# Optimization experiments

Measured on AMD Instinct MI355X. Metric: run time of the kernel, lower is better.

Reference implementation:

```python
import jax, jax.numpy as jnp
import numpy as np

IN_DIM, D_MODEL, HIDDEN, N_BLOCKS, N_CLASSES = 784, 16, 6, 4, 10
BATCH = 65536


def setup_inputs() -> dict:
    key = jax.random.key(0)
    ks = jax.random.split(key, 6)
    std = 0.02
    x = jax.random.normal(ks[0], (BATCH, IN_DIM), dtype=jnp.float32)
    # nn.Linear stores weight as [out, in]; we keep that convention.
    W_embed = jax.random.normal(ks[1], (D_MODEL, IN_DIM), dtype=jnp.float32) * std
    L_w = jax.random.normal(ks[2], (N_BLOCKS, HIDDEN, D_MODEL), dtype=jnp.float32) * std
    R_w = jax.random.normal(ks[3], (N_BLOCKS, HIDDEN, D_MODEL), dtype=jnp.float32) * std
    D_w = jax.random.normal(ks[4], (N_BLOCKS, D_MODEL, HIDDEN), dtype=jnp.float32) * std
    W_head = jax.random.normal(ks[5], (N_CLASSES, D_MODEL), dtype=jnp.float32) * std
    return {"x": x, "W_embed": W_embed, "L_w": L_w, "R_w": R_w, "D_w": D_w, "W_head": W_head}


def reference(x, W_embed, L_w, R_w, D_w, W_head):
    # embed: [B, in_dim] @ [in_dim, d_model]
    h_x = x @ W_embed.T  # [B, d_model]
    all_h = []
    for i in range(N_BLOCKS):  # n_blocks is a small structural constant
        u = h_x @ L_w[i].T  # [B, hidden]
        v = h_x @ R_w[i].T  # [B, hidden]
        h = u * v
        h_x = h_x + h @ D_w[i].T  # residual
        all_h.append(h)
    logits = h_x @ W_head.T  # [B, n_classes]
    return (logits, *all_h)
```

## Files before the change

kernel.cpp:

```cpp
#include <hip/hip_runtime.h>


#define IN_DIM   784
#define D_MODEL  16
#define HIDDEN   6
#define N_BLOCKS 4
#define N_CLS    10
#define BATCH    65536
#define SEG      196
#define NIT      49

__global__ __launch_bounds__(256, 4) void bilinear_resnet_fused(
    const float* __restrict__ x,
    const float* __restrict__ W_embed,
    const float* __restrict__ L_w,
    const float* __restrict__ R_w,
    const float* __restrict__ D_w,
    const float* __restrict__ W_head,
    float* __restrict__ out)
{
    __shared__ float parts[3][64][17];

    const int tid  = threadIdx.x;
    const int lane = tid & 63;
    const int wv   = __builtin_amdgcn_readfirstlane(tid >> 6);
    const int row  = blockIdx.x * 64 + lane;

    const float4* xr = reinterpret_cast<const float4*>(
        x + (size_t)row * IN_DIM + wv * SEG);
    const float* wseg = W_embed + wv * SEG;

    float acc[D_MODEL];
#pragma unroll
    for (int d = 0; d < D_MODEL; ++d) acc[d] = 0.f;

    float4 cur = xr[0];
    for (int it = 0; it < NIT; ++it) {
        float4 nxt = make_float4(0.f, 0.f, 0.f, 0.f);
        if (it + 1 < NIT) nxt = xr[it + 1];
        const float* wk = wseg + it * 4;
#pragma unroll
        for (int d = 0; d < D_MODEL; ++d) {
            const float* wd = wk + d * IN_DIM;
            float s = acc[d];
            s = fmaf(cur.x, wd[0], s);
            s = fmaf(cur.y, wd[1], s);
            s = fmaf(cur.z, wd[2], s);
            s = fmaf(cur.w, wd[3], s);
            acc[d] = s;
        }
        cur = nxt;
    }

    if (wv != 0) {
#pragma unroll
        for (int d = 0; d < D_MODEL; ++d) parts[wv - 1][lane][d] = acc[d];
    }
    __syncthreads();
    if (wv != 0) return;

#pragma unroll
    for (int d = 0; d < D_MODEL; ++d)
        acc[d] += parts[0][lane][d] + parts[1][lane][d] + parts[2][lane][d];

#pragma unroll
    for (int b = 0; b < N_BLOCKS; ++b) {
        const float* Lb = L_w + b * HIDDEN * D_MODEL;
        const float* Rb = R_w + b * HIDDEN * D_MODEL;
        const float* Db = D_w + b * D_MODEL * HIDDEN;
        float h[HIDDEN];
#pragma unroll
        for (int j = 0; j < HIDDEN; ++j) {
            float u = 0.f, v = 0.f;
#pragma unroll
            for (int d = 0; d < D_MODEL; ++d) {
                u = fmaf(acc[d], Lb[j * D_MODEL + d], u);
                v = fmaf(acc[d], Rb[j * D_MODEL + d], v);
            }
            h[j] = u * v;
        }
#pragma unroll
        for (int d = 0; d < D_MODEL; ++d) {
            float s = acc[d];
#pragma unroll
            for (int j = 0; j < HIDDEN; ++j) s = fmaf(h[j], Db[d * HIDDEN + j], s);
            acc[d] = s;
        }
        float* hout = out + (size_t)N_CLS * BATCH + (size_t)b * HIDDEN * BATCH
                      + (size_t)row * HIDDEN;
#pragma unroll
        for (int j = 0; j < HIDDEN; ++j) hout[j] = h[j];
    }

    float* lout = out + (size_t)row * N_CLS;
#pragma unroll
    for (int k = 0; k < N_CLS; ++k) {
        float s = 0.f;
#pragma unroll
        for (int d = 0; d < D_MODEL; ++d) s = fmaf(acc[d], W_head[k * D_MODEL + d], s);
        lout[k] = s;
    }
}

extern "C" void kernel_launch(void* const* d_in, const int* in_sizes, int n_in,
                              void* d_out, int out_size, void* d_ws, size_t ws_size,
                              hipStream_t stream) {
    const float* x       = (const float*)d_in[0];
    const float* W_embed = (const float*)d_in[1];
    const float* L_w     = (const float*)d_in[2];
    const float* R_w     = (const float*)d_in[3];
    const float* D_w     = (const float*)d_in[4];
    const float* W_head  = (const float*)d_in[5];
    float* out = (float*)d_out;

    const int grid = BATCH / 64;
    bilinear_resnet_fused<<<grid, 256, 0, stream>>>(
        x, W_embed, L_w, R_w, D_w, W_head, out);
}
```

Baseline: 354.2 us.

## Stage x tiles through swizzled shared memory with coalesced double-buffered loads

Replaces the per-thread strided row reads of x, where each lane read a 196-float segment of its own row, with cooperative coalesced float4 loads of 64x64 chunks into an XOR-swizzled, double-buffered LDS tile. Each wave then consumes a 16-column slice of every chunk from shared memory. The final 16 columns are read directly from global memory. The aim is better DRAM coalescing on this memory-bound embedding, at the cost of a __syncthreads per chunk and 32KB of LDS per block, which may reduce occupancy.

```diff
diff --git a/kernel.cpp b/kernel.cpp
--- a/kernel.cpp
+++ b/kernel.cpp
@@ -7,8 +7,7 @@
 #define N_BLOCKS 4
 #define N_CLS    10
 #define BATCH    65536
-#define SEG      196
-#define NIT      49
+#define NCHUNK   12
 
 __global__ __launch_bounds__(256, 4) void bilinear_resnet_fused(
     const float* __restrict__ x,
@@ -19,49 +18,99 @@
     const float* __restrict__ W_head,
     float* __restrict__ out)
 {
-    __shared__ float parts[3][64][17];
+    __shared__ float4 buf[2][64 * 16];
 
     const int tid  = threadIdx.x;
     const int lane = tid & 63;
     const int wv   = __builtin_amdgcn_readfirstlane(tid >> 6);
     const int row  = blockIdx.x * 64 + lane;
 
-    const float4* xr = reinterpret_cast<const float4*>(
-        x + (size_t)row * IN_DIM + wv * SEG);
-    const float* wseg = W_embed + wv * SEG;
+    const float* xtile = x + (size_t)blockIdx.x * 64 * IN_DIM;
 
     float acc[D_MODEL];
 #pragma unroll
     for (int d = 0; d < D_MODEL; ++d) acc[d] = 0.f;
 
-    float4 cur = xr[0];
-    for (int it = 0; it < NIT; ++it) {
-        float4 nxt = make_float4(0.f, 0.f, 0.f, 0.f);
-        if (it + 1 < NIT) nxt = xr[it + 1];
-        const float* wk = wseg + it * 4;
+    int lr[4], lk[4];
+#pragma unroll
+    for (int it = 0; it < 4; ++it) {
+        int i = it * 256 + tid;
+        lr[it] = i >> 4;
+        lk[it] = i & 15;
+    }
+
+    float4 pf[4];
+#pragma unroll
+    for (int it = 0; it < 4; ++it)
+        pf[it] = *reinterpret_cast<const float4*>(
+            xtile + (size_t)lr[it] * IN_DIM + lk[it] * 4);
+#pragma unroll
+    for (int it = 0; it < 4; ++it)
+        buf[0][lr[it] * 16 + (lk[it] ^ (lr[it] & 15))] = pf[it];
+    __syncthreads();
+
+    for (int c = 0; c < NCHUNK; ++c) {
+        if (c + 1 < NCHUNK) {
+#pragma unroll
+            for (int it = 0; it < 4; ++it)
+                pf[it] = *reinterpret_cast<const float4*>(
+                    xtile + (size_t)lr[it] * IN_DIM + (c + 1) * 64 + lk[it] * 4);
+        }
+        const float* wc = W_embed + c * 64 + wv * 16;
+        const float4* bsrc = buf[c & 1];
+#pragma unroll
+        for (int j = 0; j < 4; ++j) {
+            const int kk = wv * 4 + j;
+            const float4 xv = bsrc[lane * 16 + (kk ^ (lane & 15))];
+#pragma unroll
+            for (int d = 0; d < D_MODEL; ++d) {
+                const float* wd = wc + d * IN_DIM + j * 4;
+                float s = acc[d];
+                s = fmaf(xv.x, wd[0], s);
+                s = fmaf(xv.y, wd[1], s);
+                s = fmaf(xv.z, wd[2], s);
+                s = fmaf(xv.w, wd[3], s);
+                acc[d] = s;
+            }
+        }
+        if (c + 1 < NCHUNK) {
+#pragma unroll
+            for (int it = 0; it < 4; ++it)
+                buf[(c + 1) & 1][lr[it] * 16 + (lk[it] ^ (lr[it] & 15))] = pf[it];
+        }
+        __syncthreads();
+    }
+
+    {
+        const float4 xv = *reinterpret_cast<const float4*>(
+            x + (size_t)row * IN_DIM + 768 + wv * 4);
+        const float* wt = W_embed + 768 + wv * 4;
 #pragma unroll
         for (int d = 0; d < D_MODEL; ++d) {
-            const float* wd = wk + d * IN_DIM;
+            const float* wd = wt + d * IN_DIM;
             float s = acc[d];
-            s = fmaf(cur.x, wd[0], s);
-            s = fmaf(cur.y, wd[1], s);
-            s = fmaf(cur.z, wd[2], s);
-            s = fmaf(cur.w, wd[3], s);
+            s = fmaf(xv.x, wd[0], s);
+            s = fmaf(xv.y, wd[1], s);
+            s = fmaf(xv.z, wd[2], s);
+            s = fmaf(xv.w, wd[3], s);
             acc[d] = s;
         }
-        cur = nxt;
     }
 
+    float* parts = reinterpret_cast<float*>(&buf[0][0]);
     if (wv != 0) {
 #pragma unroll
-        for (int d = 0; d < D_MODEL; ++d) parts[wv - 1][lane][d] = acc[d];
+        for (int d = 0; d < D_MODEL; ++d)
+            parts[((wv - 1) * 64 + lane) * 17 + d] = acc[d];
     }
     __syncthreads();
     if (wv != 0) return;
 
 #pragma unroll
     for (int d = 0; d < D_MODEL; ++d)
-        acc[d] += parts[0][lane][d] + parts[1][lane][d] + parts[2][lane][d];
+        acc[d] += parts[(0 * 64 + lane) * 17 + d]
+                + parts[(1 * 64 + lane) * 17 + d]
+                + parts[(2 * 64 + lane) * 17 + d];
 
 #pragma unroll
     for (int b = 0; b < N_BLOCKS; ++b) {
```

Measured after the change: 364.4 us. +2.9%, slower.

## Compute embedding GEMM with bf16 MFMA and async double-buffered LDS staging

Applied to the files above, without the earlier changes.

Replaces the per-thread scalar FMA embedding, which split K across four waves, with an MFMA 16x16x32 bf16 matrix multiply. Each wave now owns 16 rows. The x tile is streamed into LDS with global_load_lds in double-buffered 64-column chunks using an XOR swizzle, and W_embed is converted to bf16 once per block into LDS. It also vectorizes the h and logits stores as float2. Rounding inputs to bf16 lowers precision, and each block re-converts W_embed on entry.

```diff
diff --git a/kernel.cpp b/kernel.cpp
--- a/kernel.cpp
+++ b/kernel.cpp
@@ -7,10 +7,22 @@
 #define N_BLOCKS 4
 #define N_CLS    10
 #define BATCH    65536
-#define SEG      196
-#define NIT      49
-
-__global__ __launch_bounds__(256, 4) void bilinear_resnet_fused(
+#define KC       64
+#define NCH      12
+#define WPITCH   808
+
+typedef const __attribute__((address_space(1))) void gvoid_t;
+typedef __attribute__((address_space(3))) void svoid_t;
+typedef __attribute__((ext_vector_type(8))) short bf16x8;
+typedef __attribute__((ext_vector_type(4))) float f32x4;
+
+__device__ __forceinline__ short f2bf(float f) {
+    unsigned u = __builtin_bit_cast(unsigned, f);
+    unsigned r = (u + 0x7FFFu + ((u >> 16) & 1u)) >> 16;
+    return (short)r;
+}
+
+__global__ __launch_bounds__(256, 2) void bilinear_resnet_fused(
     const float* __restrict__ x,
     const float* __restrict__ W_embed,
     const float* __restrict__ L_w,
@@ -19,49 +31,113 @@
     const float* __restrict__ W_head,
     float* __restrict__ out)
 {
-    __shared__ float parts[3][64][17];
+    __shared__ float4 xbuf[2][64 * 16];
+    __shared__ short  Wlds[16 * WPITCH];
+    __shared__ float4 xtail[64 * 4];
+    __shared__ float  hx[64 * 20];
 
     const int tid  = threadIdx.x;
     const int lane = tid & 63;
     const int wv   = __builtin_amdgcn_readfirstlane(tid >> 6);
-    const int row  = blockIdx.x * 64 + lane;
-
-    const float4* xr = reinterpret_cast<const float4*>(
-        x + (size_t)row * IN_DIM + wv * SEG);
-    const float* wseg = W_embed + wv * SEG;
-
-    float acc[D_MODEL];
-#pragma unroll
-    for (int d = 0; d < D_MODEL; ++d) acc[d] = 0.f;
-
-    float4 cur = xr[0];
-    for (int it = 0; it < NIT; ++it) {
-        float4 nxt = make_float4(0.f, 0.f, 0.f, 0.f);
-        if (it + 1 < NIT) nxt = xr[it + 1];
-        const float* wk = wseg + it * 4;
-#pragma unroll
-        for (int d = 0; d < D_MODEL; ++d) {
-            const float* wd = wk + d * IN_DIM;
-            float s = acc[d];
-            s = fmaf(cur.x, wd[0], s);
-            s = fmaf(cur.y, wd[1], s);
-            s = fmaf(cur.z, wd[2], s);
-            s = fmaf(cur.w, wd[3], s);
-            acc[d] = s;
-        }
-        cur = nxt;
-    }
-
-    if (wv != 0) {
-#pragma unroll
-        for (int d = 0; d < D_MODEL; ++d) parts[wv - 1][lane][d] = acc[d];
+    const char* xtile = (const char*)(x + (size_t)blockIdx.x * 64 * IN_DIM);
+
+    for (int d = 0; d < D_MODEL; ++d) {
+#pragma unroll
+        for (int c0 = 0; c0 < WPITCH; c0 += 256) {
+            int c = c0 + tid;
+            if (c < WPITCH) {
+                float v = (c < IN_DIM) ? W_embed[d * IN_DIM + c] : 0.f;
+                Wlds[d * WPITCH + c] = f2bf(v);
+            }
+        }
+    }
+
+    auto stage = [&](int c, int b) {
+#pragma unroll
+        for (int i = 0; i < 4; ++i) {
+            const int ii = wv * 4 + i;
+            const int r  = ii * 4 + (lane >> 4);
+            const int q  = (lane & 15) ^ (r & 7);
+            const char* src = xtile + (size_t)r * (IN_DIM * 4) + c * (KC * 4) + q * 16;
+            char* dst = (char*)&xbuf[b][ii * 64];
+            __builtin_amdgcn_global_load_lds((gvoid_t*)src, (svoid_t*)dst, 16, 0, 0);
+        }
+    };
+    auto stage_tail = [&]() {
+        const int r = wv * 16 + (lane >> 2);
+        const int p = lane & 3;
+        const char* src = xtile + (size_t)r * (IN_DIM * 4) + 768 * 4 + p * 16;
+        char* dst = (char*)&xtail[wv * 64];
+        __builtin_amdgcn_global_load_lds((gvoid_t*)src, (svoid_t*)dst, 16, 0, 0);
+    };
+
+    stage(0, 0);
+    __syncthreads();
+
+    const int m = lane & 15;
+    const int g = lane >> 4;
+    const int mrow = wv * 16 + m;
+
+    f32x4 acc = {0.f, 0.f, 0.f, 0.f};
+
+    for (int c = 0; c < NCH; ++c) {
+        if (c + 1 < NCH) stage(c + 1, (c + 1) & 1);
+        else             stage_tail();
+
+        const float4* xb = &xbuf[c & 1][0];
+#pragma unroll
+        for (int ks = 0; ks < 2; ++ks) {
+            const int q0 = ks * 8 + 2 * g;
+            const int p0 = q0 ^ (m & 7);
+            const float4 a0 = xb[mrow * 16 + p0];
+            const float4 a1 = xb[mrow * 16 + (p0 ^ 1)];
+            bf16x8 af;
+            af[0] = f2bf(a0.x); af[1] = f2bf(a0.y);
+            af[2] = f2bf(a0.z); af[3] = f2bf(a0.w);
+            af[4] = f2bf(a1.x); af[5] = f2bf(a1.y);
+            af[6] = f2bf(a1.z); af[7] = f2bf(a1.w);
+            const bf16x8 bf = *(const bf16x8*)&Wlds[m * WPITCH + c * KC + ks * 32 + g * 8];
+            acc = __builtin_amdgcn_mfma_f32_16x16x32_bf16(af, bf, acc, 0, 0, 0);
+        }
+        __syncthreads();
+    }
+
+    {
+        bf16x8 af;
+        if (g < 2) {
+            const float4 a0 = xtail[mrow * 4 + g * 2];
+            const float4 a1 = xtail[mrow * 4 + g * 2 + 1];
+            af[0] = f2bf(a0.x); af[1] = f2bf(a0.y);
+            af[2] = f2bf(a0.z); af[3] = f2bf(a0.w);
+            af[4] = f2bf(a1.x); af[5] = f2bf(a1.y);
+            af[6] = f2bf(a1.z); af[7] = f2bf(a1.w);
+        } else {
+#pragma unroll
+            for (int j = 0; j < 8; ++j) af[j] = 0;
+        }
+        const bf16x8 bf = *(const bf16x8*)&Wlds[m * WPITCH + 768 + g * 8];
+        acc = __builtin_amdgcn_mfma_f32_16x16x32_bf16(af, bf, acc, 0, 0, 0);
+    }
+
+    {
+        const int rbase = wv * 16 + g * 4;
+#pragma unroll
+        for (int r = 0; r < 4; ++r)
+            hx[(rbase + r) * 20 + m] = acc[r];
     }
     __syncthreads();
     if (wv != 0) return;
 
-#pragma unroll
-    for (int d = 0; d < D_MODEL; ++d)
-        acc[d] += parts[0][lane][d] + parts[1][lane][d] + parts[2][lane][d];
+    const int row = blockIdx.x * 64 + lane;
+    float hxr[D_MODEL];
+    {
+        const float4* hp = (const float4*)&hx[lane * 20];
+        const float4 t0 = hp[0], t1 = hp[1], t2 = hp[2], t3 = hp[3];
+        hxr[0]=t0.x; hxr[1]=t0.y; hxr[2]=t0.z; hxr[3]=t0.w;
+        hxr[4]=t1.x; hxr[5]=t1.y; hxr[6]=t1.z; hxr[7]=t1.w;
+        hxr[8]=t2.x; hxr[9]=t2.y; hxr[10]=t2.z; hxr[11]=t2.w;
+        hxr[12]=t3.x; hxr[13]=t3.y; hxr[14]=t3.z; hxr[15]=t3.w;
+    }
 
 #pragma unroll
     for (int b = 0; b < N_BLOCKS; ++b) {
@@ -74,31 +150,37 @@
             float u = 0.f, v = 0.f;
 #pragma unroll
             for (int d = 0; d < D_MODEL; ++d) {
-                u = fmaf(acc[d], Lb[j * D_MODEL + d], u);
-                v = fmaf(acc[d], Rb[j * D_MODEL + d], v);
+                u = fmaf(hxr[d], Lb[j * D_MODEL + d], u);
+                v = fmaf(hxr[d], Rb[j * D_MODEL + d], v);
             }
             h[j] = u * v;
         }
 #pragma unroll
         for (int d = 0; d < D_MODEL; ++d) {
-            float s = acc[d];
+            float s = hxr[d];
 #pragma unroll
             for (int j = 0; j < HIDDEN; ++j) s = fmaf(h[j], Db[d * HIDDEN + j], s);
-            acc[d] = s;
+            hxr[d] = s;
         }
         float* hout = out + (size_t)N_CLS * BATCH + (size_t)b * HIDDEN * BATCH
                       + (size_t)row * HIDDEN;
-#pragma unroll
-        for (int j = 0; j < HIDDEN; ++j) hout[j] = h[j];
+        const float2 h01 = {h[0], h[1]}, h23 = {h[2], h[3]}, h45 = {h[4], h[5]};
+        ((float2*)hout)[0] = h01;
+        ((float2*)hout)[1] = h23;
+        ((float2*)hout)[2] = h45;
     }
 
     float* lout = out + (size_t)row * N_CLS;
 #pragma unroll
-    for (int k = 0; k < N_CLS; ++k) {
-        float s = 0.f;
-#pragma unroll
-        for (int d = 0; d < D_MODEL; ++d) s = fmaf(acc[d], W_head[k * D_MODEL + d], s);
-        lout[k] = s;
+    for (int k = 0; k < N_CLS; k += 2) {
+        float s0 = 0.f, s1 = 0.f;
+#pragma unroll
+        for (int d = 0; d < D_MODEL; ++d) {
+            s0 = fmaf(hxr[d], W_head[k * D_MODEL + d], s0);
+            s1 = fmaf(hxr[d], W_head[(k + 1) * D_MODEL + d], s1);
+        }
+        const float2 s = {s0, s1};
+        ((float2*)lout)[k >> 1] = s;
     }
 }
 
```

Measured after the change: 340.2 us. 3.9% less time.
